# Kernel optimization log

Hardware: AMD Instinct MI355X
Metric: run time of the kernel (lower is better)

## Reference

```python
import jax, jax.numpy as jnp
import numpy as np

NUM_BANDS, B, K, D = 5, 512, 64, 200
H = 4            # num attention heads
HID = 512        # selector hidden width
S = 0.02         # weight init scale


def setup_inputs() -> dict:
    key = jax.random.key(0)
    ks = jax.random.split(key, 8)
    F_IN = NUM_BANDS * K * D  # 64000
    return {
        "bands": jax.random.normal(ks[0], (NUM_BANDS, B, K, D), jnp.float32),
        "w1": jax.random.normal(ks[1], (HID, F_IN), jnp.float32) * S,
        "b1": jnp.zeros((HID,), jnp.float32),
        "w2": jax.random.normal(ks[2], (NUM_BANDS, HID), jnp.float32) * S,
        "b2": jnp.zeros((NUM_BANDS,), jnp.float32),
        "in_proj_w": jax.random.normal(ks[3], (3 * D, D), jnp.float32) * S,
        "in_proj_b": jnp.zeros((3 * D,), jnp.float32),
        "out_w": jax.random.normal(ks[4], (D, D), jnp.float32) * S,
        "out_b": jnp.zeros((D,), jnp.float32),
    }


def reference(bands, w1, b1, w2, b2, in_proj_w, in_proj_b, out_w, out_b):
    nb, Bb, k, d = bands.shape
    hd = d // H
    scale = 1.0 / np.sqrt(hd)

    # concat(bands, dim=1): [B, nb*k, d] in band-major order
    x = jnp.transpose(bands, (1, 0, 2, 3))           # [B, nb, k, d]
    kv_in = x.reshape(Bb, nb * k, d)                 # [B, nb*k, d]

    # router MLP + softmax + argmax band select
    flat = kv_in.reshape(Bb, -1)                     # [B, nb*k*d]
    h = jax.nn.relu(flat @ w1.T + b1)                # [B, HID]
    band_weights = jax.nn.softmax(h @ w2.T + b2, axis=-1)
    sel = jnp.argmax(band_weights, axis=-1)          # [B] int

    # gather selected band per sample as the query
    Q = bands[sel, jnp.arange(Bb)]                   # [B, k, d]

    # multihead cross-attention (torch nn.MultiheadAttention math)
    wq, wk, wv = jnp.split(in_proj_w, 3, axis=0)
    bq, bk, bv = jnp.split(in_proj_b, 3, axis=0)
    q = (Q @ wq.T + bq).reshape(Bb, k, H, hd).transpose(0, 2, 1, 3)        # [B,H,k,hd]
    kk = (kv_in @ wk.T + bk).reshape(Bb, nb * k, H, hd).transpose(0, 2, 1, 3)
    v = (kv_in @ wv.T + bv).reshape(Bb, nb * k, H, hd).transpose(0, 2, 1, 3)

    attn = jax.nn.softmax(jnp.einsum('bhqe,bhke->bhqk', q, kk) * scale, axis=-1)
    o = jnp.einsum('bhqk,bhke->bhqe', attn, v)       # [B,H,k,hd]
    o = o.transpose(0, 2, 1, 3).reshape(Bb, k, d)
    return o @ out_w.T + out_b                        # [B, k, d]
```

## Files before the change

### kernel.cpp

```cpp
#include <hip/hip_runtime.h>
#include <hip/hip_bf16.h>

#define NBANDS 5
#define BATCH  512
#define KQN    64
#define DM     200
#define NHEAD  4
#define HD     50
#define HIDW   512
#define TKV    320
#define FIN    64000
#define BSTRIDE 6553600
#define KSPLIT 40
#define KCH    1600
#define RC32   50
#define NTT    13
#define KST    7
#define NTKV   25

typedef __bf16  bf16x8 __attribute__((ext_vector_type(8)));
typedef float   f32x4  __attribute__((ext_vector_type(4)));

static __device__ inline unsigned short f2bf(float f) {
    __hip_bfloat16 h = __float2bfloat16(f);
    return *reinterpret_cast<unsigned short*>(&h);
}
static __device__ inline float bf2f(unsigned short u) {
    union { unsigned int i; float f; } x;
    x.i = ((unsigned int)u) << 16;
    return x.f;
}
static __device__ inline bf16x8 bf8zero() {
    union { bf16x8 v; unsigned int u[4]; } z;
    z.u[0] = z.u[1] = z.u[2] = z.u[3] = 0u;
    return z.v;
}
static __device__ inline void split8(const float4& a, const float4& b,
                                     bf16x8& hi, bf16x8& lo) {
    union { bf16x8 v; unsigned short u[8]; } H, L;
    const float xs[8] = {a.x, a.y, a.z, a.w, b.x, b.y, b.z, b.w};
#pragma unroll
    for (int i = 0; i < 8; ++i) {
        H.u[i] = f2bf(xs[i]);
        L.u[i] = f2bf(xs[i] - bf2f(H.u[i]));
    }
    hi = H.v; lo = L.v;
}
static __device__ inline bf16x8 round8(const float4& a, const float4& b) {
    union { bf16x8 v; unsigned short u[8]; } H;
    const float xs[8] = {a.x, a.y, a.z, a.w, b.x, b.y, b.z, b.w};
#pragma unroll
    for (int i = 0; i < 8; ++i) H.u[i] = f2bf(xs[i]);
    return H.v;
}

__global__ __launch_bounds__(256) void k_splitw1(
    const float* __restrict__ w1, unsigned short* __restrict__ BHp,
    unsigned short* __restrict__ BLp)
{
    __shared__ __align__(16) unsigned short Hs[128][72];
    __shared__ __align__(16) unsigned short Ls[128][72];
    const int kc = blockIdx.x;
    const int jt = blockIdx.y;
    const int t  = threadIdx.x;
    const int rl0 = t >> 4, cl4 = (t & 15) * 4;
#pragma unroll
    for (int i = 0; i < 8; ++i) {
        const int row = rl0 + i * 16;
        const float4 v = *(const float4*)(w1
            + (size_t)(jt * 128 + row) * FIN + kc * 64 + cl4);
        ushort4 hh, ll;
        hh.x = f2bf(v.x); ll.x = f2bf(v.x - bf2f(hh.x));
        hh.y = f2bf(v.y); ll.y = f2bf(v.y - bf2f(hh.y));
        hh.z = f2bf(v.z); ll.z = f2bf(v.z - bf2f(hh.z));
        hh.w = f2bf(v.w); ll.w = f2bf(v.w - bf2f(hh.w));
        *(ushort4*)&Hs[row][cl4] = hh;
        *(ushort4*)&Ls[row][cl4] = ll;
    }
    __syncthreads();
    const size_t tbase = ((size_t)(jt * 1000 + kc)) << 13;
#pragma unroll
    for (int i = 0; i < 4; ++i) {
        const int slot = i * 256 + t;
        const int ksnt = slot >> 6, lane = slot & 63;
        const int ks = ksnt >> 3, nt = ksnt & 7;
        const int row = nt * 16 + (lane & 15);
        const int col = ks * 32 + (lane >> 4) * 8;
        *(uint4*)(BHp + tbase + (size_t)slot * 8) = *(const uint4*)&Hs[row][col];
        *(uint4*)(BLp + tbase + (size_t)slot * 8) = *(const uint4*)&Ls[row][col];
    }
}

__global__ __launch_bounds__(256, 3) void k_router_mfma(
    const float* __restrict__ bands, const unsigned short* __restrict__ BHp,
    const unsigned short* __restrict__ BLp, float* __restrict__ part)
{
    __shared__ __align__(16) unsigned short BsH[2][4096];
    __shared__ __align__(16) unsigned short BsL[2][4096];

    const int lin = (blockIdx.z << 4) | (blockIdx.y << 2) | blockIdx.x;
    const int logical = (lin & 7) * 80 + (lin >> 3);
    const int z   = logical >> 4;
    const int rem = logical & 15;
    const int bt  = rem >> 2, jt = rem & 3;

    const int t = threadIdx.x;
    const int w = t >> 6, lane = t & 63;
    const int lm = lane & 15, quad = lane >> 4;
    const int wr = w >> 1, wc = w & 1;

    const float* xbase = bands + (size_t)(z >> 3) * BSTRIDE
                       + (size_t)(bt * 128 + wr * 64 + lm) * 12800
                       + (z & 7) * KCH + quad * 8;
    const unsigned short* hbase = BHp + ((size_t)(jt * 1000 + z * 25) << 13);
    const unsigned short* lbase = BLp + ((size_t)(jt * 1000 + z * 25) << 13);

    auto stage = [&](int c, int buf) {
        const size_t off = ((size_t)(c >> 1) << 13) + ((size_t)(c & 1) << 12);
        const unsigned short* sH = hbase + off;
        const unsigned short* sL = lbase + off;
#pragma unroll
        for (int pass = 0; pass < 2; ++pass) {
            const int i = pass * 256 + t;
            __builtin_amdgcn_global_load_lds(
                (const __attribute__((address_space(1))) unsigned int*)(sH + (size_t)i * 8),
                (__attribute__((address_space(3))) unsigned int*)&BsH[buf][(pass * 256 + w * 64) * 8],
                16, 0, 0);
            __builtin_amdgcn_global_load_lds(
                (const __attribute__((address_space(1))) unsigned int*)(sL + (size_t)i * 8),
                (__attribute__((address_space(3))) unsigned int*)&BsL[buf][(pass * 256 + w * 64) * 8],
                16, 0, 0);
        }
    };

    f32x4 acc[4][4];
#pragma unroll
    for (int rs = 0; rs < 4; ++rs)
#pragma unroll
        for (int nt = 0; nt < 4; ++nt) acc[rs][nt] = (f32x4){0.f, 0.f, 0.f, 0.f};

    stage(0, 0);
    __syncthreads();
    for (int c = 0; c < RC32; ++c) {
        const int buf = c & 1;
        if (c + 1 < RC32) stage(c + 1, buf ^ 1);
        float4 a0[4], a1[4];
#pragma unroll
        for (int rs = 0; rs < 4; ++rs) {
            const float* ap = xbase + (size_t)(rs * 16) * 12800 + c * 32;
            a0[rs] = *(const float4*)(ap);
            a1[rs] = *(const float4*)(ap + 4);
        }
        bf16x8 ah[4], al[4];
#pragma unroll
        for (int rs = 0; rs < 4; ++rs) split8(a0[rs], a1[rs], ah[rs], al[rs]);
        const unsigned short* hc = &BsH[buf][(wc * 4) * 512 + lane * 8];
        const unsigned short* lc = &BsL[buf][(wc * 4) * 512 + lane * 8];
#pragma unroll
        for (int nt = 0; nt < 4; ++nt) {
            const bf16x8 bh = *(const bf16x8*)(hc + (nt << 9));
            const bf16x8 bl = *(const bf16x8*)(lc + (nt << 9));
#pragma unroll
            for (int rs = 0; rs < 4; ++rs) {
                acc[rs][nt] = __builtin_amdgcn_mfma_f32_16x16x32_bf16(ah[rs], bh, acc[rs][nt], 0, 0, 0);
                acc[rs][nt] = __builtin_amdgcn_mfma_f32_16x16x32_bf16(al[rs], bh, acc[rs][nt], 0, 0, 0);
                acc[rs][nt] = __builtin_amdgcn_mfma_f32_16x16x32_bf16(ah[rs], bl, acc[rs][nt], 0, 0, 0);
            }
        }
        __syncthreads();
    }
    float* po = part + (size_t)z * (BATCH * HIDW);
    const int j0 = jt * 128 + wc * 64;
    const int b0 = bt * 128 + wr * 64;
#pragma unroll
    for (int rs = 0; rs < 4; ++rs) {
#pragma unroll
        for (int nt = 0; nt < 4; ++nt) {
            const int jj = j0 + nt * 16 + lm;
#pragma unroll
            for (int reg = 0; reg < 4; ++reg) {
                const int bb = b0 + rs * 16 + quad * 4 + reg;
                po[(size_t)bb * HIDW + jj] = acc[rs][nt][reg];
            }
        }
    }
}

__global__ __launch_bounds__(256) void k_reduce_relu(
    const float* __restrict__ part, const float* __restrict__ b1,
    float* __restrict__ h)
{
    const int tid = blockIdx.x * 256 + threadIdx.x;
    float s = b1[tid & (HIDW - 1)];
#pragma unroll 8
    for (int z = 0; z < KSPLIT; ++z) s += part[z * (BATCH * HIDW) + tid];
    h[tid] = fmaxf(s, 0.f);
}

__global__ __launch_bounds__(256) void k_wpack(
    const float* __restrict__ ipw, const float* __restrict__ outw,
    unsigned short* __restrict__ WqHp, unsigned short* __restrict__ WqLp,
    unsigned short* __restrict__ OwHp, unsigned short* __restrict__ OwLp)
{
    const int p = blockIdx.x;
    const int ks = p / NTT, nt = p - ks * NTT;
    const int t = threadIdx.x;
    const int lane = t >> 2, e0 = (t & 3) * 2;
    const int lm = lane & 15, quad = lane >> 4;
    const int row = nt * 16 + lm;
    const int k  = ks * 32 + quad * 8 + e0;
    const float* src = (blockIdx.y == 0) ? ipw : outw;
    unsigned short* dh = (blockIdx.y == 0) ? WqHp : OwHp;
    unsigned short* dl = (blockIdx.y == 0) ? WqLp : OwLp;
    float v0 = 0.f, v1 = 0.f;
    if (row < DM && k < DM) {
        v0 = src[(size_t)row * DM + k];
        v1 = src[(size_t)row * DM + k + 1];
    }
    const int off = (p << 9) + (lane << 3) + e0;
    const unsigned short h0 = f2bf(v0), h1 = f2bf(v1);
    dh[off]     = h0;
    dh[off + 1] = h1;
    dl[off]     = f2bf(v0 - bf2f(h0));
    dl[off + 1] = f2bf(v1 - bf2f(h1));
}

__global__ __launch_bounds__(256) void k_wpack_kv(
    const float* __restrict__ ipw, unsigned short* __restrict__ Wkv)
{
    const int p = blockIdx.x;
    const int ks = p / NTKV, nt = p - ks * NTKV;
    const int t = threadIdx.x;
    const int lane = t >> 2, e0 = (t & 3) * 2;
    const int lm = lane & 15, quad = lane >> 4;
    const int row = nt * 16 + lm;
    const int k  = ks * 32 + quad * 8 + e0;
    float v0 = 0.f, v1 = 0.f;
    if (k < DM) {
        v0 = ipw[(size_t)(DM + row) * DM + k];
        v1 = ipw[(size_t)(DM + row) * DM + k + 1];
    }
    const int off = (p << 9) + (lane << 3) + e0;
    Wkv[off]     = f2bf(v0);
    Wkv[off + 1] = f2bf(v1);
}

__global__ __launch_bounds__(256) void k_argmax(
    const float* __restrict__ h, const float* __restrict__ w2,
    const float* __restrict__ b2, int* __restrict__ sel)
{
    __shared__ float red[NBANDS][256];
    const int b = blockIdx.x, t = threadIdx.x;
    float acc[NBANDS] = {0.f, 0.f, 0.f, 0.f, 0.f};
    for (int j = t; j < HIDW; j += 256) {
        const float hv = h[b * HIDW + j];
#pragma unroll
        for (int n = 0; n < NBANDS; ++n)
            acc[n] = fmaf(hv, w2[n * HIDW + j], acc[n]);
    }
#pragma unroll
    for (int n = 0; n < NBANDS; ++n) red[n][t] = acc[n];
    __syncthreads();
    for (int s = 128; s > 0; s >>= 1) {
        if (t < s) {
#pragma unroll
            for (int n = 0; n < NBANDS; ++n) red[n][t] += red[n][t + s];
        }
        __syncthreads();
    }
    if (t == 0) {
        int best = 0;
        float bv = red[0][0] + b2[0];
        for (int n = 1; n < NBANDS; ++n) {
            const float v = red[n][0] + b2[n];
            if (v > bv) { bv = v; best = n; }
        }
        sel[b] = best;
    }
}

template<bool BF16OUT>
static __device__ inline void proj_core(
    const float* __restrict__ x0,
    const unsigned short* __restrict__ Ph,
    const unsigned short* __restrict__ Pl,
    const float* __restrict__ bias,
    void* __restrict__ outp)
{
    const int t = threadIdx.x;
    const int w = t >> 6, lane = t & 63;
    const int lm = lane & 15, quad = lane >> 4;
    const int m0 = w * 16;
    const float* xrow = x0 + (size_t)(m0 + lm) * DM;

    f32x4 acc[NTT];
#pragma unroll
    for (int nt = 0; nt < NTT; ++nt) acc[nt] = (f32x4){0.f, 0.f, 0.f, 0.f};

#pragma unroll
    for (int ks = 0; ks < KST; ++ks) {
        const int k0 = ks * 32 + quad * 8;
        bf16x8 a_h = bf8zero(), a_l = bf8zero();
        if (k0 + 8 <= DM) {
            const float4 xa = *(const float4*)(xrow + k0);
            const float4 xb = *(const float4*)(xrow + k0 + 4);
            split8(xa, xb, a_h, a_l);
        }
        const unsigned short* ph = Ph + ((ks * NTT) << 9) + (lane << 3);
        const unsigned short* pl = Pl + ((ks * NTT) << 9) + (lane << 3);
#pragma unroll
        for (int nt = 0; nt < NTT; ++nt) {
            const bf16x8 b_h = *(const bf16x8*)(ph + (nt << 9));
            const bf16x8 b_l = *(const bf16x8*)(pl + (nt << 9));
            acc[nt] = __builtin_amdgcn_mfma_f32_16x16x32_bf16(a_h, b_h, acc[nt], 0, 0, 0);
            acc[nt] = __builtin_amdgcn_mfma_f32_16x16x32_bf16(a_l, b_h, acc[nt], 0, 0, 0);
            acc[nt] = __builtin_amdgcn_mfma_f32_16x16x32_bf16(a_h, b_l, acc[nt], 0, 0, 0);
        }
    }
#pragma unroll
    for (int nt = 0; nt < NTT; ++nt) {
        const int col = nt * 16 + lm;
        if (col < DM) {
            const float bs = bias[col];
#pragma unroll
            for (int reg = 0; reg < 4; ++reg) {
                const int row = m0 + quad * 4 + reg;
                const float v = acc[nt][reg] + bs;
                if (BF16OUT)
                    ((unsigned short*)outp)[(size_t)row * DM + col] = f2bf(v);
                else
                    ((float*)outp)[(size_t)row * DM + col] = v;
            }
        }
    }
}

__global__ __launch_bounds__(256) void k_qproj_mfma(
    const float* __restrict__ bands, const int* __restrict__ sel,
    const unsigned short* __restrict__ WqHp, const unsigned short* __restrict__ WqLp,
    const float* __restrict__ ipb, unsigned short* __restrict__ qb)
{
    const int b = blockIdx.x;
    const int band = sel[b];
    const float* x0 = bands + (size_t)((band * BATCH + b) * KQN) * DM;
    proj_core<true>(x0, WqHp, WqLp, ipb, qb + (size_t)(b * KQN) * DM);
}

__global__ __launch_bounds__(256) void k_outproj_mfma(
    const float* __restrict__ obuf, const unsigned short* __restrict__ OwHp,
    const unsigned short* __restrict__ OwLp, const float* __restrict__ outb,
    float* __restrict__ out)
{
    const int b = blockIdx.x;
    proj_core<false>(obuf + (size_t)(b * KQN) * DM, OwHp, OwLp, outb,
                     out + (size_t)(b * KQN) * DM);
}

__global__ __launch_bounds__(256) void k_kvproj_lds(
    const float* __restrict__ bands, const unsigned short* __restrict__ Wkv,
    const float* __restrict__ ipb, __hip_bfloat16* __restrict__ Kp,
    __hip_bfloat16* __restrict__ Vp)
{
    __shared__ __align__(16) unsigned short Bs[2][NTKV * 512];
    const int t = threadIdx.x;
    const int w = t >> 6, lane = t & 63;
    const int lm = lane & 15, quad = lane >> 4;
    const int m0 = w * 16;
    const int M0 = blockIdx.x * 64;

    const int gg = M0 + m0 + lm;
    const int bb = gg / TKV, tk = gg - bb * TKV;
    const int band = tk >> 6, kk = tk & 63;
    const float* xrow = bands + (size_t)((band * BATCH + bb) * KQN + kk) * DM;

    float4 ar[2 * KST];
#pragma unroll
    for (int ks = 0; ks < KST; ++ks) {
        const int k0 = ks * 32 + quad * 8;
        if (k0 + 8 <= DM) {
            ar[2 * ks]     = *(const float4*)(xrow + k0);
            ar[2 * ks + 1] = *(const float4*)(xrow + k0 + 4);
        }
    }
    bf16x8 a[KST];
#pragma unroll
    for (int ks = 0; ks < KST; ++ks) {
        const int k0 = ks * 32 + quad * 8;
        a[ks] = (k0 + 8 <= DM) ? round8(ar[2 * ks], ar[2 * ks + 1]) : bf8zero();
    }

    auto stage = [&](int ks, int buf) {
        const unsigned short* src = Wkv + ((ks * NTKV) << 9);
#pragma unroll
        for (int pass = 0; pass < 6; ++pass) {
            const int i = pass * 256 + t;
            __builtin_amdgcn_global_load_lds(
                (const __attribute__((address_space(1))) unsigned int*)(src + (size_t)i * 8),
                (__attribute__((address_space(3))) unsigned int*)&Bs[buf][(pass * 256 + w * 64) * 8],
                16, 0, 0);
        }
        if (t < 64) {
            __builtin_amdgcn_global_load_lds(
                (const __attribute__((address_space(1))) unsigned int*)(src + (size_t)(1536 + lane) * 8),
                (__attribute__((address_space(3))) unsigned int*)&Bs[buf][1536 * 8],
                16, 0, 0);
        }
    };

    f32x4 acc[NTKV];
#pragma unroll
    for (int nt = 0; nt < NTKV; ++nt) acc[nt] = (f32x4){0.f, 0.f, 0.f, 0.f};

    stage(0, 0);
    __syncthreads();
#pragma unroll
    for (int ks = 0; ks < KST; ++ks) {
        if (ks + 1 < KST) stage(ks + 1, (ks + 1) & 1);
        const unsigned short* bs = &Bs[ks & 1][lane * 8];
#pragma unroll
        for (int nt = 0; nt < NTKV; ++nt) {
            const bf16x8 b8 = *(const bf16x8*)(bs + (nt << 9));
            acc[nt] = __builtin_amdgcn_mfma_f32_16x16x32_bf16(a[ks], b8, acc[nt], 0, 0, 0);
        }
        __syncthreads();
    }

#pragma unroll
    for (int nt = 0; nt < NTKV; ++nt) {
        const int col = nt * 16 + lm;
        const float bias = ipb[DM + col];
#pragma unroll
        for (int reg = 0; reg < 4; ++reg) {
            const int grow = M0 + m0 + quad * 4 + reg;
            const float v = acc[nt][reg] + bias;
            if (col < DM) Kp[(size_t)grow * DM + col] = __float2bfloat16(v);
            else          Vp[(size_t)grow * DM + (col - DM)] = __float2bfloat16(v);
        }
    }
}

__global__ __launch_bounds__(256) void k_attn(
    const unsigned short* __restrict__ qb, const __hip_bfloat16* __restrict__ Kp,
    const __hip_bfloat16* __restrict__ Vp, float* __restrict__ obuf)
{
    __shared__ __align__(16) unsigned short Qs[64][72];
    __shared__ __align__(16) unsigned short KP[320][72];
    __shared__ __align__(16) unsigned short Vt[64][328];
    __shared__ __align__(16) unsigned short Ps[64][328];
    const int b = blockIdx.x, hh = blockIdx.y;
    const int t = threadIdx.x;

    const unsigned short* qbase = qb + (size_t)(b * KQN) * DM + hh * HD;
    for (int idx = t; idx < 64 * 64; idx += 256) {
        const int r = idx >> 6, e = idx & 63;
        Qs[r][e] = (e < HD) ? qbase[(size_t)r * DM + e] : 0;
    }
    const unsigned short* kbase = (const unsigned short*)Kp + (size_t)b * TKV * DM + hh * HD;
    for (int idx = t; idx < 320 * 25; idx += 256) {
        const int key = idx / 25, g = idx - key * 25;
        *(unsigned int*)&KP[key][g * 2] =
            *(const unsigned int*)(kbase + (size_t)key * DM + g * 2);
    }
    for (int idx = t; idx < 320 * 7; idx += 256) {
        const int key = idx / 7, g = idx - key * 7;
        *(unsigned int*)&KP[key][50 + g * 2] = 0;
    }
    const unsigned short* vbase = (const unsigned short*)Vp + (size_t)b * TKV * DM + hh * HD;
    for (int idx = t; idx < 320 * 25; idx += 256) {
        const int key = idx / 25, g = idx - key * 25;
        const unsigned int v = *(const unsigned int*)(vbase + (size_t)key * DM + g * 2);
        Vt[g * 2][key]     = (unsigned short)(v & 0xffffu);
        Vt[g * 2 + 1][key] = (unsigned short)(v >> 16);
    }
    __syncthreads();

    const int w = t >> 6, lane = t & 63;
    const int lm = lane & 15, quad = lane >> 4;
    const int m0 = w * 16;

    f32x4 s[20];
#pragma unroll
    for (int nt = 0; nt < 20; ++nt) s[nt] = (f32x4){0.f, 0.f, 0.f, 0.f};
#pragma unroll
    for (int ks = 0; ks < 2; ++ks) {
        const int ka = ks * 32 + quad * 8;
        const bf16x8 a = *(const bf16x8*)&Qs[m0 + lm][ka];
#pragma unroll
        for (int nt = 0; nt < 20; ++nt) {
            const bf16x8 bb8 = *(const bf16x8*)&KP[nt * 16 + lm][ka];
            s[nt] = __builtin_amdgcn_mfma_f32_16x16x32_bf16(a, bb8, s[nt], 0, 0, 0);
        }
    }

    const float scale = 0.14142135623730951f;
    float inv[4];
#pragma unroll
    for (int reg = 0; reg < 4; ++reg) {
        float mx = -1e30f;
#pragma unroll
        for (int nt = 0; nt < 20; ++nt) {
            const float sv = s[nt][reg] * scale;
            s[nt][reg] = sv;
            mx = fmaxf(mx, sv);
        }
#pragma unroll
        for (int off = 1; off < 16; off <<= 1)
            mx = fmaxf(mx, __shfl_xor(mx, off, 64));
        float lsum = 0.f;
#pragma unroll
        for (int nt = 0; nt < 20; ++nt) {
            const float p = __expf(s[nt][reg] - mx);
            s[nt][reg] = p;
            lsum += p;
        }
#pragma unroll
        for (int off = 1; off < 16; off <<= 1)
            lsum += __shfl_xor(lsum, off, 64);
        inv[reg] = 1.f / lsum;
    }
#pragma unroll
    for (int reg = 0; reg < 4; ++reg) {
        const int row = m0 + quad * 4 + reg;
#pragma unroll
        for (int nt = 0; nt < 20; ++nt)
            Ps[row][nt * 16 + lm] = f2bf(s[nt][reg]);
    }
    __syncthreads();

    f32x4 o[4];
#pragma unroll
    for (int nt = 0; nt < 4; ++nt) o[nt] = (f32x4){0.f, 0.f, 0.f, 0.f};
#pragma unroll
    for (int ks = 0; ks < 10; ++ks) {
        const int ka = ks * 32 + quad * 8;
        const bf16x8 a = *(const bf16x8*)&Ps[m0 + lm][ka];
#pragma unroll
        for (int nt = 0; nt < 4; ++nt) {
            const bf16x8 bb8 = *(const bf16x8*)&Vt[nt * 16 + lm][ka];
            o[nt] = __builtin_amdgcn_mfma_f32_16x16x32_bf16(a, bb8, o[nt], 0, 0, 0);
        }
    }
    float* op = obuf + (size_t)(b * KQN) * DM + hh * HD;
#pragma unroll
    for (int nt = 0; nt < 4; ++nt) {
        const int e = nt * 16 + lm;
        if (e < HD) {
#pragma unroll
            for (int reg = 0; reg < 4; ++reg) {
                const int row = m0 + quad * 4 + reg;
                op[(size_t)row * DM + e] = o[nt][reg] * inv[reg];
            }
        }
    }
}

extern "C" void kernel_launch(void* const* d_in, const int* in_sizes, int n_in,
                              void* d_out, int out_size, void* d_ws, size_t ws_size,
                              hipStream_t stream)
{
    const float* bands = (const float*)d_in[0];
    const float* w1    = (const float*)d_in[1];
    const float* b1    = (const float*)d_in[2];
    const float* w2    = (const float*)d_in[3];
    const float* b2    = (const float*)d_in[4];
    const float* ipw   = (const float*)d_in[5];
    const float* ipb   = (const float*)d_in[6];
    const float* outw  = (const float*)d_in[7];
    const float* outb  = (const float*)d_in[8];
    float* out = (float*)d_out;

    if (ws_size < (size_t)192940032) return;

    char* ws = (char*)d_ws;
    int*   sel  = (int*)  (ws + 0);
    unsigned short* BHp  = (unsigned short*)(ws + 4096);
    unsigned short* BLp  = (unsigned short*)(ws + 65540096);
    float* part = (float*)(ws + 131076096);
    float* h    = (float*)(ws + 173019136);
    unsigned short* qb   = (unsigned short*)(ws + 4096);
    __hip_bfloat16* Kp   = (__hip_bfloat16*)(ws + 26776832);
    __hip_bfloat16* Vp   = (__hip_bfloat16*)(ws + 92312832);
    float* obuf = (float*)(ws + 157848832);
    unsigned short* Wkv  = (unsigned short*)(ws + 184063232);
    unsigned short* WqHp = (unsigned short*)(ws + 184242432);
    unsigned short* WqLp = (unsigned short*)(ws + 184335616);
    unsigned short* OwHp = (unsigned short*)(ws + 184428800);
    unsigned short* OwLp = (unsigned short*)(ws + 184521984);

    k_wpack_kv<<<KST * NTKV, 256, 0, stream>>>(ipw, Wkv);
    k_wpack<<<dim3(KST * NTT, 2), 256, 0, stream>>>(ipw, outw, WqHp, WqLp, OwHp, OwLp);
    k_splitw1<<<dim3(1000, 4), 256, 0, stream>>>(w1, BHp, BLp);

    k_router_mfma<<<dim3(4, 4, KSPLIT), 256, 0, stream>>>(bands, BHp, BLp, part);
    k_reduce_relu<<<(BATCH * HIDW) / 256, 256, 0, stream>>>(part, b1, h);
    k_argmax<<<BATCH, 256, 0, stream>>>(h, w2, b2, sel);
    k_qproj_mfma<<<BATCH, 256, 0, stream>>>(bands, sel, WqHp, WqLp, ipb, qb);
    k_kvproj_lds<<<2560, 256, 0, stream>>>(bands, Wkv, ipb, Kp, Vp);
    k_attn<<<dim3(BATCH, NHEAD), 256, 0, stream>>>(qb, Kp, Vp, obuf);
    k_outproj_mfma<<<BATCH, 256, 0, stream>>>(obuf, OwHp, OwLp, outb, out);
}
```

Before: 861.0 us.

## Enlarge router GEMM tiles to 256x256 with A staged through LDS

```diff
diff --git a/kernel.cpp b/kernel.cpp
--- a/kernel.cpp
+++ b/kernel.cpp
@@ -11,9 +11,9 @@
 #define TKV    320
 #define FIN    64000
 #define BSTRIDE 6553600
-#define KSPLIT 40
-#define KCH    1600
-#define RC32   50
+#define KSPLIT 50
+#define KCH    1280
+#define NCH    40
 #define NTT    13
 #define KST    7
 #define NTKV   25
@@ -91,89 +91,115 @@
     }
 }
 
-__global__ __launch_bounds__(256, 3) void k_router_mfma(
+__global__ __launch_bounds__(512, 2) void k_router_mfma(
     const float* __restrict__ bands, const unsigned short* __restrict__ BHp,
     const unsigned short* __restrict__ BLp, float* __restrict__ part)
 {
-    __shared__ __align__(16) unsigned short BsH[2][4096];
-    __shared__ __align__(16) unsigned short BsL[2][4096];
-
-    const int lin = (blockIdx.z << 4) | (blockIdx.y << 2) | blockIdx.x;
-    const int logical = (lin & 7) * 80 + (lin >> 3);
-    const int z   = logical >> 4;
-    const int rem = logical & 15;
-    const int bt  = rem >> 2, jt = rem & 3;
+    __shared__ __align__(16) unsigned short BsH[2][8192];
+    __shared__ __align__(16) unsigned short BsL[2][8192];
+    __shared__ __align__(16) unsigned short Ah[8192];
+    __shared__ __align__(16) unsigned short Al[8192];
+
+    const int lin = (blockIdx.z << 2) | (blockIdx.y << 1) | blockIdx.x;
+    const int logical = (lin & 7) * 25 + (lin >> 3);
+    const int z   = logical >> 2;
+    const int rem = logical & 3;
+    const int bt  = rem >> 1, jt = rem & 1;
 
     const int t = threadIdx.x;
     const int w = t >> 6, lane = t & 63;
     const int lm = lane & 15, quad = lane >> 4;
-    const int wr = w >> 1, wc = w & 1;
-
-    const float* xbase = bands + (size_t)(z >> 3) * BSTRIDE
-                       + (size_t)(bt * 128 + wr * 64 + lm) * 12800
-                       + (z & 7) * KCH + quad * 8;
-    const unsigned short* hbase = BHp + ((size_t)(jt * 1000 + z * 25) << 13);
-    const unsigned short* lbase = BLp + ((size_t)(jt * 1000 + z * 25) << 13);
-
-    auto stage = [&](int c, int buf) {
-        const size_t off = ((size_t)(c >> 1) << 13) + ((size_t)(c & 1) << 12);
-        const unsigned short* sH = hbase + off;
-        const unsigned short* sL = lbase + off;
-#pragma unroll
-        for (int pass = 0; pass < 2; ++pass) {
-            const int i = pass * 256 + t;
+    const int wr = w >> 2, wc = w & 3;
+
+    const float* abase = bands + (size_t)(z / 10) * BSTRIDE
+                       + (size_t)(bt * 256 + w * 32 + lm) * 12800
+                       + (z % 10) * KCH + quad * 8;
+
+    auto stageB = [&](int c, int buf) {
+        const int kc = z * 20 + (c >> 1);
+        const int ks = c & 1;
+#pragma unroll
+        for (int p = 0; p < 4; ++p) {
+            const int plane = p >> 1, r = p & 1;
+            const unsigned short* src = (plane ? BLp : BHp)
+                + ((size_t)((jt * 2 + r) * 1000 + kc) << 13) + (ks << 12)
+                + (size_t)t * 8;
+            unsigned short* dst = (plane ? &BsL[buf][0] : &BsH[buf][0])
+                + (r << 12) + ((t >> 6) << 9);
             __builtin_amdgcn_global_load_lds(
-                (const __attribute__((address_space(1))) unsigned int*)(sH + (size_t)i * 8),
-                (__attribute__((address_space(3))) unsigned int*)&BsH[buf][(pass * 256 + w * 64) * 8],
-                16, 0, 0);
-            __builtin_amdgcn_global_load_lds(
-                (const __attribute__((address_space(1))) unsigned int*)(sL + (size_t)i * 8),
-                (__attribute__((address_space(3))) unsigned int*)&BsL[buf][(pass * 256 + w * 64) * 8],
-                16, 0, 0);
+                (const __attribute__((address_space(1))) unsigned int*)src,
+                (__attribute__((address_space(3))) unsigned int*)dst, 16, 0, 0);
         }
     };
 
-    f32x4 acc[4][4];
-#pragma unroll
-    for (int rs = 0; rs < 4; ++rs)
+    float4 ar[4];
+    auto loadA = [&](int c) {
+        const float* ap = abase + c * 32;
+        ar[0] = *(const float4*)(ap);
+        ar[1] = *(const float4*)(ap + 4);
+        ar[2] = *(const float4*)(ap + (size_t)16 * 12800);
+        ar[3] = *(const float4*)(ap + (size_t)16 * 12800 + 4);
+    };
+    auto writeA = [&]() {
+        bf16x8 h0, l0, h1, l1;
+        split8(ar[0], ar[1], h0, l0);
+        split8(ar[2], ar[3], h1, l1);
+        *(bf16x8*)&Ah[(w * 2 + 0) * 512 + lane * 8] = h0;
+        *(bf16x8*)&Al[(w * 2 + 0) * 512 + lane * 8] = l0;
+        *(bf16x8*)&Ah[(w * 2 + 1) * 512 + lane * 8] = h1;
+        *(bf16x8*)&Al[(w * 2 + 1) * 512 + lane * 8] = l1;
+    };
+
+    f32x4 acc[8][4];
+#pragma unroll
+    for (int rs = 0; rs < 8; ++rs)
 #pragma unroll
         for (int nt = 0; nt < 4; ++nt) acc[rs][nt] = (f32x4){0.f, 0.f, 0.f, 0.f};
 
-    stage(0, 0);
+    loadA(0);
+    stageB(0, 0);
     __syncthreads();
-    for (int c = 0; c < RC32; ++c) {
-        const int buf = c & 1;
-        if (c + 1 < RC32) stage(c + 1, buf ^ 1);
-        float4 a0[4], a1[4];
-#pragma unroll
-        for (int rs = 0; rs < 4; ++rs) {
-            const float* ap = xbase + (size_t)(rs * 16) * 12800 + c * 32;
-            a0[rs] = *(const float4*)(ap);
-            a1[rs] = *(const float4*)(ap + 4);
-        }
-        bf16x8 ah[4], al[4];
-#pragma unroll
-        for (int rs = 0; rs < 4; ++rs) split8(a0[rs], a1[rs], ah[rs], al[rs]);
-        const unsigned short* hc = &BsH[buf][(wc * 4) * 512 + lane * 8];
-        const unsigned short* lc = &BsL[buf][(wc * 4) * 512 + lane * 8];
+    writeA();
+    __syncthreads();
+
+    for (int c = 0; c < NCH; ++c) {
+        if (c + 1 < NCH) {
+            stageB(c + 1, (c + 1) & 1);
+            loadA(c + 1);
+        }
+        const unsigned short* bh = &BsH[c & 1][(wc * 4) * 512 + lane * 8];
+        const unsigned short* bl = &BsL[c & 1][(wc * 4) * 512 + lane * 8];
+        const unsigned short* ahp = &Ah[(wr * 8) * 512 + lane * 8];
+        const unsigned short* alp = &Al[(wr * 8) * 512 + lane * 8];
+        bf16x8 bhv[4], blv[4];
 #pragma unroll
         for (int nt = 0; nt < 4; ++nt) {
-            const bf16x8 bh = *(const bf16x8*)(hc + (nt << 9));
-            const bf16x8 bl = *(const bf16x8*)(lc + (nt << 9));
-#pragma unroll
-            for (int rs = 0; rs < 4; ++rs) {
-                acc[rs][nt] = __builtin_amdgcn_mfma_f32_16x16x32_bf16(ah[rs], bh, acc[rs][nt], 0, 0, 0);
-                acc[rs][nt] = __builtin_amdgcn_mfma_f32_16x16x32_bf16(al[rs], bh, acc[rs][nt], 0, 0, 0);
-                acc[rs][nt] = __builtin_amdgcn_mfma_f32_16x16x32_bf16(ah[rs], bl, acc[rs][nt], 0, 0, 0);
+            bhv[nt] = *(const bf16x8*)(bh + nt * 512);
+            blv[nt] = *(const bf16x8*)(bl + nt * 512);
+        }
+#pragma unroll
+        for (int rs = 0; rs < 8; ++rs) {
+            const bf16x8 a_h = *(const bf16x8*)(ahp + rs * 512);
+            const bf16x8 a_l = *(const bf16x8*)(alp + rs * 512);
+#pragma unroll
+            for (int nt = 0; nt < 4; ++nt) {
+                acc[rs][nt] = __builtin_amdgcn_mfma_f32_16x16x32_bf16(a_h, bhv[nt], acc[rs][nt], 0, 0, 0);
+                acc[rs][nt] = __builtin_amdgcn_mfma_f32_16x16x32_bf16(a_l, bhv[nt], acc[rs][nt], 0, 0, 0);
+                acc[rs][nt] = __builtin_amdgcn_mfma_f32_16x16x32_bf16(a_h, blv[nt], acc[rs][nt], 0, 0, 0);
             }
         }
         __syncthreads();
-    }
+        if (c + 1 < NCH) {
+            writeA();
+        }
+        __syncthreads();
+    }
+
     float* po = part + (size_t)z * (BATCH * HIDW);
-    const int j0 = jt * 128 + wc * 64;
-    const int b0 = bt * 128 + wr * 64;
-#pragma unroll
-    for (int rs = 0; rs < 4; ++rs) {
+    const int j0 = jt * 256 + wc * 64;
+    const int b0 = bt * 256 + wr * 128;
+#pragma unroll
+    for (int rs = 0; rs < 8; ++rs) {
 #pragma unroll
         for (int nt = 0; nt < 4; ++nt) {
             const int jj = j0 + nt * 16 + lm;
@@ -192,7 +218,7 @@
 {
     const int tid = blockIdx.x * 256 + threadIdx.x;
     float s = b1[tid & (HIDW - 1)];
-#pragma unroll 8
+#pragma unroll 10
     for (int z = 0; z < KSPLIT; ++z) s += part[z * (BATCH * HIDW) + tid];
     h[tid] = fmaxf(s, 0.f);
 }
@@ -576,22 +602,22 @@
     unsigned short* BHp  = (unsigned short*)(ws + 4096);
     unsigned short* BLp  = (unsigned short*)(ws + 65540096);
     float* part = (float*)(ws + 131076096);
-    float* h    = (float*)(ws + 173019136);
+    float* h    = (float*)(ws + 183504896);
     unsigned short* qb   = (unsigned short*)(ws + 4096);
     __hip_bfloat16* Kp   = (__hip_bfloat16*)(ws + 26776832);
     __hip_bfloat16* Vp   = (__hip_bfloat16*)(ws + 92312832);
     float* obuf = (float*)(ws + 157848832);
-    unsigned short* Wkv  = (unsigned short*)(ws + 184063232);
-    unsigned short* WqHp = (unsigned short*)(ws + 184242432);
-    unsigned short* WqLp = (unsigned short*)(ws + 184335616);
-    unsigned short* OwHp = (unsigned short*)(ws + 184428800);
-    unsigned short* OwLp = (unsigned short*)(ws + 184521984);
+    unsigned short* Wkv  = (unsigned short*)(ws + 184553472);
+    unsigned short* WqHp = (unsigned short*)(ws + 184732672);
+    unsigned short* WqLp = (unsigned short*)(ws + 184825856);
+    unsigned short* OwHp = (unsigned short*)(ws + 184919040);
+    unsigned short* OwLp = (unsigned short*)(ws + 185012224);
 
     k_wpack_kv<<<KST * NTKV, 256, 0, stream>>>(ipw, Wkv);
     k_wpack<<<dim3(KST * NTT, 2), 256, 0, stream>>>(ipw, outw, WqHp, WqLp, OwHp, OwLp);
     k_splitw1<<<dim3(1000, 4), 256, 0, stream>>>(w1, BHp, BLp);
 
-    k_router_mfma<<<dim3(4, 4, KSPLIT), 256, 0, stream>>>(bands, BHp, BLp, part);
+    k_router_mfma<<<dim3(2, 2, KSPLIT), 512, 0, stream>>>(bands, BHp, BLp, part);
     k_reduce_relu<<<(BATCH * HIDW) / 256, 256, 0, stream>>>(part, b1, h);
     k_argmax<<<BATCH, 256, 0, stream>>>(h, w2, b2, sel);
     k_qproj_mfma<<<BATCH, 256, 0, stream>>>(bands, sel, WqHp, WqLp, ipb, qb);
```

Measured after the change: 813.0 us. -5.6%, faster.
